# Performance work log

Hardware: AMD Instinct MI355X
Metric: run time of the kernel (lower is better)

## Reference

```python
import jax, jax.numpy as jnp
import numpy as np

C, H, W = 512, 192, 192  # feature map dims; 3x3 patches at stride 3 (non-overlapping)


def setup_inputs() -> dict:
    key = jax.random.key(0)
    k1, k2 = jax.random.split(key)
    model_resp = jax.random.normal(k1, (1, C, H, W), dtype=jnp.float32)
    style_resp = jax.random.normal(k2, (1, C, H, W), dtype=jnp.float32)
    return {"model_resp": model_resp, "style_resp": style_resp}


def _unfold3(x):
    # torch.nn.Unfold(kernel=3, stride=3) on (1, C, H, W) -> (C*9, L) after the
    # module's view(patch_count, patch_size) (note: rows are feature channels,
    # columns are spatial locations, matching the original code's dim order).
    _, c, h, w = x.shape
    p = x[0].reshape(c, h // 3, 3, w // 3, 3)          # (c, ph, kh, pw, kw)
    p = p.transpose(0, 2, 4, 1, 3)                      # (c, kh, kw, ph, pw)
    return p.reshape(c * 9, (h // 3) * (w // 3))        # (A, L)


def reference(model_resp, style_resp):
    img = _unfold3(model_resp)                          # (A, L)
    sty = _unfold3(style_resp)                          # (A, L)
    img_norm = 1.0 / jnp.linalg.norm(img, axis=1)       # (A,)
    sty_norm = 1.0 / jnp.linalg.norm(sty, axis=1)       # (A,)
    S = img @ sty.T                                     # (A, A), S[i,j] = img_i . sty_j
    # Faithful to torch: expand(A, A) of a 1-D tensor broadcasts along dim 0,
    # i.e. multiplies COLUMNS by the normalizer vector.
    S1 = S * img_norm[None, :]
    S2 = S1.T * sty_norm[None, :]                       # S2[i,j] = img_norm[i]*sty_norm[j]*(img_j . sty_i)
    nearest = jnp.argmax(S2, axis=0)                    # (A,) int
    max_sim = jnp.max(S2, axis=0)                       # (A,) float (the online-max values)
    return nearest, max_sim
```

## Files before the change

### kernel.cpp

```cpp
#include <hip/hip_runtime.h>
#include <hip/hip_bf16.h>
#include <hip/hip_fp16.h>

#define A_DIM 4608
#define L_DIM 4096
#define CH    512
#define H_DIM 192
#define W_DIM 192

typedef _Float16 half8 __attribute__((ext_vector_type(8)));
typedef float   floatx4 __attribute__((ext_vector_type(4)));
typedef float   floatx16 __attribute__((ext_vector_type(16)));

__global__ __launch_bounds__(256) void prep_kernel(
    const float* __restrict__ x0, const float* __restrict__ x1,
    _Float16* __restrict__ Uhi0, _Float16* __restrict__ Ulo0,
    _Float16* __restrict__ Uhi1, _Float16* __restrict__ Ulo1,
    float* __restrict__ nr0, float* __restrict__ nr1) {
  const int which = blockIdx.z;
  const float* __restrict__ x = which ? x1 : x0;
  _Float16* __restrict__ Uhi = which ? Uhi1 : Uhi0;
  _Float16* __restrict__ Ulo = which ? Ulo1 : Ulo0;
  float* __restrict__ nrecip = which ? nr1 : nr0;

  const int c = blockIdx.x, kh = blockIdx.y;
  const int a0 = c * 9 + kh * 3;
  const float* __restrict__ xb = x + (size_t)c * (H_DIM * W_DIM) + kh * W_DIM;
  const int t = threadIdx.x;

  float ss0 = 0.f, ss1 = 0.f, ss2 = 0.f;
#pragma unroll
  for (int it = 0; it < 16; ++it) {
    const int l = it * 256 + t;
    const int ph = l >> 6, pw = l & 63;
    const float* __restrict__ p = xb + (3 * ph) * W_DIM + 3 * pw;
    const float v0 = p[0], v1 = p[1], v2 = p[2];
    ss0 += v0 * v0; ss1 += v1 * v1; ss2 += v2 * v2;
    const _Float16 h0 = (_Float16)v0, h1 = (_Float16)v1, h2 = (_Float16)v2;
    Uhi[(size_t)(a0 + 0) * L_DIM + l] = h0;
    Uhi[(size_t)(a0 + 1) * L_DIM + l] = h1;
    Uhi[(size_t)(a0 + 2) * L_DIM + l] = h2;
    Ulo[(size_t)(a0 + 0) * L_DIM + l] = (_Float16)(v0 - (float)h0);
    Ulo[(size_t)(a0 + 1) * L_DIM + l] = (_Float16)(v1 - (float)h1);
    Ulo[(size_t)(a0 + 2) * L_DIM + l] = (_Float16)(v2 - (float)h2);
  }
  __shared__ float wss[3][4];
  const int wid = t >> 6, lane = t & 63;
  float s[3] = {ss0, ss1, ss2};
#pragma unroll
  for (int kw = 0; kw < 3; ++kw) {
    float v = s[kw];
#pragma unroll
    for (int off = 32; off > 0; off >>= 1) v += __shfl_down(v, off, 64);
    if (lane == 0) wss[kw][wid] = v;
  }
  __syncthreads();
  if (t < 3) {
    const float tot = wss[t][0] + wss[t][1] + wss[t][2] + wss[t][3];
    nrecip[a0 + t] = 1.0f / sqrtf(tot);
  }
}

#define GLDS(g, l)                                                          \
  __builtin_amdgcn_global_load_lds(                                        \
      (const __attribute__((address_space(1))) void*)(g),                   \
      (__attribute__((address_space(3))) void*)(l), 16, 0, 0)

__global__ __launch_bounds__(256) void gemm_max_kernel(
    const _Float16* __restrict__ Shi, const _Float16* __restrict__ Slo,
    const _Float16* __restrict__ Ihi, const _Float16* __restrict__ Ilo,
    const float* __restrict__ img_nr,
    unsigned long long* __restrict__ packed) {
  __shared__ _Float16 sAh[128 * 32];
  __shared__ _Float16 sAl[128 * 32];
  __shared__ _Float16 sBh[128 * 32];
  __shared__ _Float16 sBl[128 * 32];

  const int t = threadIdx.x;
  const int lane = t & 63, wv = t >> 6;
  const int wr = wv >> 1, wc = wv & 1;
  const int row0 = blockIdx.y * 128;
  const int col0 = blockIdx.x * 128;
  const int l31 = lane & 31, hs = lane >> 5;

  floatx16 acc[2][2];
#pragma unroll
  for (int rf = 0; rf < 2; ++rf)
#pragma unroll
    for (int cf = 0; cf < 2; ++cf) acc[rf][cf] = (floatx16)0.f;

  const int sr = t >> 2;
  const int sseg = (t & 3) ^ ((t >> 3) & 3);
  const size_t rskip = (size_t)64 * L_DIM;
  const _Float16* pAh = Shi + (size_t)(row0 + sr) * L_DIM + sseg * 8;
  const _Float16* pAl = Slo + (size_t)(row0 + sr) * L_DIM + sseg * 8;
  const _Float16* pBh = Ihi + (size_t)(col0 + sr) * L_DIM + sseg * 8;
  const _Float16* pBl = Ilo + (size_t)(col0 + sr) * L_DIM + sseg * 8;
  const int lofs = t * 8;

  int aoff[2][2], boff[2][2];
#pragma unroll
  for (int rf = 0; rf < 2; ++rf)
#pragma unroll
    for (int kk = 0; kk < 2; ++kk) {
      const int ar = wr * 64 + rf * 32 + l31;
      const int as = kk * 2 + hs;
      aoff[rf][kk] = (ar * 4 + (as ^ ((ar >> 1) & 3))) * 8;
      const int br = wc * 64 + rf * 32 + l31;
      boff[rf][kk] = (br * 4 + (as ^ ((br >> 1) & 3))) * 8;
    }

  for (int k0 = 0; k0 < L_DIM; k0 += 32) {
    __syncthreads();
    GLDS(pAh,         &sAh[lofs]);
    GLDS(pAh + rskip, &sAh[lofs + 2048]);
    GLDS(pAl,         &sAl[lofs]);
    GLDS(pAl + rskip, &sAl[lofs + 2048]);
    GLDS(pBh,         &sBh[lofs]);
    GLDS(pBh + rskip, &sBh[lofs + 2048]);
    GLDS(pBl,         &sBl[lofs]);
    GLDS(pBl + rskip, &sBl[lofs + 2048]);
    pAh += 32; pAl += 32; pBh += 32; pBl += 32;
    __syncthreads();

    half8 ah[2][2], al[2][2], bh[2][2], bl[2][2];
#pragma unroll
    for (int rf = 0; rf < 2; ++rf)
#pragma unroll
      for (int kk = 0; kk < 2; ++kk) {
        ah[rf][kk] = *(const half8*)&sAh[aoff[rf][kk]];
        al[rf][kk] = *(const half8*)&sAl[aoff[rf][kk]];
        bh[rf][kk] = *(const half8*)&sBh[boff[rf][kk]];
        bl[rf][kk] = *(const half8*)&sBl[boff[rf][kk]];
      }
#pragma unroll
    for (int rf = 0; rf < 2; ++rf)
#pragma unroll
      for (int cf = 0; cf < 2; ++cf)
#pragma unroll
        for (int kk = 0; kk < 2; ++kk) {
          acc[rf][cf] = __builtin_amdgcn_mfma_f32_32x32x16_f16(
              ah[rf][kk], bh[cf][kk], acc[rf][cf], 0, 0, 0);
          acc[rf][cf] = __builtin_amdgcn_mfma_f32_32x32x16_f16(
              ah[rf][kk], bl[cf][kk], acc[rf][cf], 0, 0, 0);
          acc[rf][cf] = __builtin_amdgcn_mfma_f32_32x32x16_f16(
              al[rf][kk], bh[cf][kk], acc[rf][cf], 0, 0, 0);
        }
  }

#pragma unroll
  for (int cf = 0; cf < 2; ++cf) {
    const int j = col0 + wc * 64 + cf * 32 + l31;
    float best = -3.4e38f;
    int bi = 0x7FFFFFFF;
#pragma unroll
    for (int rf = 0; rf < 2; ++rf) {
      const int base_i = row0 + wr * 64 + rf * 32 + 4 * hs;
#pragma unroll
      for (int g = 0; g < 4; ++g) {
        const floatx4 n4 = *(const floatx4*)&img_nr[base_i + 8 * g];
#pragma unroll
        for (int r = 0; r < 4; ++r) {
          const int i = base_i + 8 * g + r;
          const float v = acc[rf][cf][g * 4 + r] * n4[r];
          if (v > best) { best = v; bi = i; }
        }
      }
    }
    const float ov = __shfl_xor(best, 32, 64);
    const int oi = __shfl_xor(bi, 32, 64);
    if (ov > best || (ov == best && oi < bi)) { best = ov; bi = oi; }
    if (hs == 0) {
      const unsigned u = __float_as_uint(best);
      const unsigned key = (u & 0x80000000u) ? ~u : (u | 0x80000000u);
      const unsigned long long pk =
          ((unsigned long long)key << 32) | (unsigned)(~(unsigned)bi);
      atomicMax(&packed[j], pk);
    }
  }
}

__global__ __launch_bounds__(256) void finalize_kernel(
    const unsigned long long* __restrict__ packed,
    const float* __restrict__ sty_nr, float* __restrict__ out) {
  const int j = blockIdx.x * 256 + threadIdx.x;
  if (j >= A_DIM) return;
  const unsigned long long p = packed[j];
  const unsigned key = (unsigned)(p >> 32);
  const unsigned u = (key & 0x80000000u) ? (key ^ 0x80000000u) : ~key;
  const float v = __uint_as_float(u);
  const int idx = (int)(~(unsigned)(p & 0xFFFFFFFFu));
  out[j] = (float)idx;
  out[A_DIM + j] = v * sty_nr[j];
}

extern "C" void kernel_launch(void* const* d_in, const int* in_sizes, int n_in,
                              void* d_out, int out_size, void* d_ws, size_t ws_size,
                              hipStream_t stream) {
  const float* model = (const float*)d_in[0];
  const float* style = (const float*)d_in[1];
  float* out = (float*)d_out;
  char* ws = (char*)d_ws;

  const size_t usz = (size_t)A_DIM * L_DIM * 2;
  _Float16* img_hi = (_Float16*)(ws);
  _Float16* img_lo = (_Float16*)(ws + usz);
  _Float16* sty_hi = (_Float16*)(ws + 2 * usz);
  _Float16* sty_lo = (_Float16*)(ws + 3 * usz);
  float* img_nr = (float*)(ws + 4 * usz);
  float* sty_nr = img_nr + A_DIM;
  unsigned long long* packed = (unsigned long long*)(img_nr + 2 * A_DIM);

  hipMemsetAsync(packed, 0, (size_t)A_DIM * 8, stream);
  prep_kernel<<<dim3(CH, 3, 2), 256, 0, stream>>>(
      model, style, img_hi, img_lo, sty_hi, sty_lo, img_nr, sty_nr);
  gemm_max_kernel<<<dim3(36, 36), 256, 0, stream>>>(sty_hi, sty_lo, img_hi,
                                                    img_lo, img_nr, packed);
  finalize_kernel<<<18, 256, 0, stream>>>(packed, sty_nr, out);
}
```

Before: 766.7 us.

## Use k-chunked operand layout and 256x128 tiles in split-fp16 GEMM

The prep kernel now writes the hi/lo fp16 operands in a layout where each 8-element K chunk is contiguous across all A rows ([L/8][A][8]). This lets the GEMM load LDS tiles with fully coalesced 16-byte rows and read fragments without swizzling. The GEMM tile grows from 128x128 to 256x128, so each wave holds 4x2 accumulators, which raises operand reuse per LDS load and cuts how often B is refetched. The costs are more registers per thread (launch bounds now ask for 2 blocks), only 18x36 blocks, and scattered 2-byte stores in prep.

```diff
diff --git a/kernel.cpp b/kernel.cpp
--- a/kernel.cpp
+++ b/kernel.cpp
@@ -7,6 +7,10 @@
 #define CH    512
 #define H_DIM 192
 #define W_DIM 192
+
+#define BM 256
+#define BN 128
+#define BK 32
 
 typedef _Float16 half8 __attribute__((ext_vector_type(8)));
 typedef float   floatx4 __attribute__((ext_vector_type(4)));
@@ -37,12 +41,13 @@
     const float v0 = p[0], v1 = p[1], v2 = p[2];
     ss0 += v0 * v0; ss1 += v1 * v1; ss2 += v2 * v2;
     const _Float16 h0 = (_Float16)v0, h1 = (_Float16)v1, h2 = (_Float16)v2;
-    Uhi[(size_t)(a0 + 0) * L_DIM + l] = h0;
-    Uhi[(size_t)(a0 + 1) * L_DIM + l] = h1;
-    Uhi[(size_t)(a0 + 2) * L_DIM + l] = h2;
-    Ulo[(size_t)(a0 + 0) * L_DIM + l] = (_Float16)(v0 - (float)h0);
-    Ulo[(size_t)(a0 + 1) * L_DIM + l] = (_Float16)(v1 - (float)h1);
-    Ulo[(size_t)(a0 + 2) * L_DIM + l] = (_Float16)(v2 - (float)h2);
+    const size_t base = ((size_t)(l >> 3) * A_DIM) * 8 + (l & 7);
+    Uhi[base + (size_t)(a0 + 0) * 8] = h0;
+    Uhi[base + (size_t)(a0 + 1) * 8] = h1;
+    Uhi[base + (size_t)(a0 + 2) * 8] = h2;
+    Ulo[base + (size_t)(a0 + 0) * 8] = (_Float16)(v0 - (float)h0);
+    Ulo[base + (size_t)(a0 + 1) * 8] = (_Float16)(v1 - (float)h1);
+    Ulo[base + (size_t)(a0 + 2) * 8] = (_Float16)(v2 - (float)h2);
   }
   __shared__ float wss[3][4];
   const int wid = t >> 6, lane = t & 63;
@@ -66,96 +71,91 @@
       (const __attribute__((address_space(1))) void*)(g),                   \
       (__attribute__((address_space(3))) void*)(l), 16, 0, 0)
 
-__global__ __launch_bounds__(256) void gemm_max_kernel(
+__global__ __launch_bounds__(256, 2) void gemm_max_kernel(
     const _Float16* __restrict__ Shi, const _Float16* __restrict__ Slo,
     const _Float16* __restrict__ Ihi, const _Float16* __restrict__ Ilo,
     const float* __restrict__ img_nr,
     unsigned long long* __restrict__ packed) {
-  __shared__ _Float16 sAh[128 * 32];
-  __shared__ _Float16 sAl[128 * 32];
-  __shared__ _Float16 sBh[128 * 32];
-  __shared__ _Float16 sBl[128 * 32];
+  __shared__ _Float16 sAh[4 * BM * 8];
+  __shared__ _Float16 sAl[4 * BM * 8];
+  __shared__ _Float16 sBh[4 * BN * 8];
+  __shared__ _Float16 sBl[4 * BN * 8];
 
   const int t = threadIdx.x;
   const int lane = t & 63, wv = t >> 6;
-  const int wr = wv >> 1, wc = wv & 1;
-  const int row0 = blockIdx.y * 128;
-  const int col0 = blockIdx.x * 128;
+  const int wvr = wv >> 1, wvc = wv & 1;
+  const int row0 = blockIdx.y * BM;
+  const int col0 = blockIdx.x * BN;
   const int l31 = lane & 31, hs = lane >> 5;
 
-  floatx16 acc[2][2];
-#pragma unroll
-  for (int rf = 0; rf < 2; ++rf)
+  floatx16 acc[4][2];
+#pragma unroll
+  for (int rf = 0; rf < 4; ++rf)
 #pragma unroll
     for (int cf = 0; cf < 2; ++cf) acc[rf][cf] = (floatx16)0.f;
 
-  const int sr = t >> 2;
-  const int sseg = (t & 3) ^ ((t >> 3) & 3);
-  const size_t rskip = (size_t)64 * L_DIM;
-  const _Float16* pAh = Shi + (size_t)(row0 + sr) * L_DIM + sseg * 8;
-  const _Float16* pAl = Slo + (size_t)(row0 + sr) * L_DIM + sseg * 8;
-  const _Float16* pBh = Ihi + (size_t)(col0 + sr) * L_DIM + sseg * 8;
-  const _Float16* pBl = Ilo + (size_t)(col0 + sr) * L_DIM + sseg * 8;
-  const int lofs = t * 8;
-
-  int aoff[2][2], boff[2][2];
-#pragma unroll
-  for (int rf = 0; rf < 2; ++rf)
+  const size_t CH8 = (size_t)A_DIM * 8;
+  const _Float16* pAh = Shi + (size_t)(row0 + t) * 8;
+  const _Float16* pAl = Slo + (size_t)(row0 + t) * 8;
+  const _Float16* pBh = Ihi + (size_t)(col0 + (t & 127)) * 8 + (size_t)(t >> 7) * CH8;
+  const _Float16* pBl = Ilo + (size_t)(col0 + (t & 127)) * 8 + (size_t)(t >> 7) * CH8;
+  const int dA = t * 8;
+
+  for (int ks = 0; ks < L_DIM / BK; ++ks) {
+    __syncthreads();
+    GLDS(pAh + 0 * CH8, &sAh[dA + 0 * 2048]);
+    GLDS(pAh + 1 * CH8, &sAh[dA + 1 * 2048]);
+    GLDS(pAh + 2 * CH8, &sAh[dA + 2 * 2048]);
+    GLDS(pAh + 3 * CH8, &sAh[dA + 3 * 2048]);
+    GLDS(pAl + 0 * CH8, &sAl[dA + 0 * 2048]);
+    GLDS(pAl + 1 * CH8, &sAl[dA + 1 * 2048]);
+    GLDS(pAl + 2 * CH8, &sAl[dA + 2 * 2048]);
+    GLDS(pAl + 3 * CH8, &sAl[dA + 3 * 2048]);
+    GLDS(pBh + 0 * CH8, &sBh[dA]);
+    GLDS(pBh + 2 * CH8, &sBh[dA + 2048]);
+    GLDS(pBl + 0 * CH8, &sBl[dA]);
+    GLDS(pBl + 2 * CH8, &sBl[dA + 2048]);
+    pAh += 4 * CH8; pAl += 4 * CH8; pBh += 4 * CH8; pBl += 4 * CH8;
+    __syncthreads();
+
 #pragma unroll
     for (int kk = 0; kk < 2; ++kk) {
-      const int ar = wr * 64 + rf * 32 + l31;
-      const int as = kk * 2 + hs;
-      aoff[rf][kk] = (ar * 4 + (as ^ ((ar >> 1) & 3))) * 8;
-      const int br = wc * 64 + rf * 32 + l31;
-      boff[rf][kk] = (br * 4 + (as ^ ((br >> 1) & 3))) * 8;
+      half8 ah[4], al[4], bh[2], bl[2];
+      const int kc = kk * 2 + hs;
+#pragma unroll
+      for (int rf = 0; rf < 4; ++rf) {
+        const int idx = (kc * BM + wvr * 128 + rf * 32 + l31) * 8;
+        ah[rf] = *(const half8*)&sAh[idx];
+        al[rf] = *(const half8*)&sAl[idx];
+      }
+#pragma unroll
+      for (int cf = 0; cf < 2; ++cf) {
+        const int idx = (kc * BN + wvc * 64 + cf * 32 + l31) * 8;
+        bh[cf] = *(const half8*)&sBh[idx];
+        bl[cf] = *(const half8*)&sBl[idx];
+      }
+#pragma unroll
+      for (int rf = 0; rf < 4; ++rf)
+#pragma unroll
+        for (int cf = 0; cf < 2; ++cf) {
+          acc[rf][cf] = __builtin_amdgcn_mfma_f32_32x32x16_f16(
+              ah[rf], bh[cf], acc[rf][cf], 0, 0, 0);
+          acc[rf][cf] = __builtin_amdgcn_mfma_f32_32x32x16_f16(
+              ah[rf], bl[cf], acc[rf][cf], 0, 0, 0);
+          acc[rf][cf] = __builtin_amdgcn_mfma_f32_32x32x16_f16(
+              al[rf], bh[cf], acc[rf][cf], 0, 0, 0);
+        }
     }
-
-  for (int k0 = 0; k0 < L_DIM; k0 += 32) {
-    __syncthreads();
-    GLDS(pAh,         &sAh[lofs]);
-    GLDS(pAh + rskip, &sAh[lofs + 2048]);
-    GLDS(pAl,         &sAl[lofs]);
-    GLDS(pAl + rskip, &sAl[lofs + 2048]);
-    GLDS(pBh,         &sBh[lofs]);
-    GLDS(pBh + rskip, &sBh[lofs + 2048]);
-    GLDS(pBl,         &sBl[lofs]);
-    GLDS(pBl + rskip, &sBl[lofs + 2048]);
-    pAh += 32; pAl += 32; pBh += 32; pBl += 32;
-    __syncthreads();
-
-    half8 ah[2][2], al[2][2], bh[2][2], bl[2][2];
-#pragma unroll
-    for (int rf = 0; rf < 2; ++rf)
-#pragma unroll
-      for (int kk = 0; kk < 2; ++kk) {
-        ah[rf][kk] = *(const half8*)&sAh[aoff[rf][kk]];
-        al[rf][kk] = *(const half8*)&sAl[aoff[rf][kk]];
-        bh[rf][kk] = *(const half8*)&sBh[boff[rf][kk]];
-        bl[rf][kk] = *(const half8*)&sBl[boff[rf][kk]];
-      }
-#pragma unroll
-    for (int rf = 0; rf < 2; ++rf)
-#pragma unroll
-      for (int cf = 0; cf < 2; ++cf)
-#pragma unroll
-        for (int kk = 0; kk < 2; ++kk) {
-          acc[rf][cf] = __builtin_amdgcn_mfma_f32_32x32x16_f16(
-              ah[rf][kk], bh[cf][kk], acc[rf][cf], 0, 0, 0);
-          acc[rf][cf] = __builtin_amdgcn_mfma_f32_32x32x16_f16(
-              ah[rf][kk], bl[cf][kk], acc[rf][cf], 0, 0, 0);
-          acc[rf][cf] = __builtin_amdgcn_mfma_f32_32x32x16_f16(
-              al[rf][kk], bh[cf][kk], acc[rf][cf], 0, 0, 0);
-        }
   }
 
 #pragma unroll
   for (int cf = 0; cf < 2; ++cf) {
-    const int j = col0 + wc * 64 + cf * 32 + l31;
+    const int j = col0 + wvc * 64 + cf * 32 + l31;
     float best = -3.4e38f;
     int bi = 0x7FFFFFFF;
 #pragma unroll
-    for (int rf = 0; rf < 2; ++rf) {
-      const int base_i = row0 + wr * 64 + rf * 32 + 4 * hs;
+    for (int rf = 0; rf < 4; ++rf) {
+      const int base_i = row0 + wvr * 128 + rf * 32 + 4 * hs;
 #pragma unroll
       for (int g = 0; g < 4; ++g) {
         const floatx4 n4 = *(const floatx4*)&img_nr[base_i + 8 * g];
@@ -214,7 +214,7 @@
   hipMemsetAsync(packed, 0, (size_t)A_DIM * 8, stream);
   prep_kernel<<<dim3(CH, 3, 2), 256, 0, stream>>>(
       model, style, img_hi, img_lo, sty_hi, sty_lo, img_nr, sty_nr);
-  gemm_max_kernel<<<dim3(36, 36), 256, 0, stream>>>(sty_hi, sty_lo, img_hi,
-                                                    img_lo, img_nr, packed);
+  gemm_max_kernel<<<dim3(A_DIM / BN, A_DIM / BM), 256, 0, stream>>>(
+      sty_hi, sty_lo, img_hi, img_lo, img_nr, packed);
   finalize_kernel<<<18, 256, 0, stream>>>(packed, sty_nr, out);
 }
```

Result: slower. 905.2 us (+18.1%).
